# Kernel optimization log

Hardware: AMD Instinct MI355X
Metric: run time of the kernel (lower is better)

The kernel has to match this reference:

```python
import jax, jax.numpy as jnp
import numpy as np

B, N, ATTR = 8, 16384, 14
G, M = 256, 32
ENC = 1024
DIM, DEPTH, HEADS = 384, 12, 6
HID = 4 * DIM
FETCH = (3, 7, 11)


def setup_inputs() -> dict:
    key = jax.random.key(0)
    ks = iter(jax.random.split(key, 40))
    def rn(shape, s=0.02):
        return jax.random.normal(next(ks), shape, dtype=jnp.float32) * s
    inp = {}
    inp["xyz"] = jax.random.normal(next(ks), (B, N, ATTR), dtype=jnp.float32)
    # T-Net: 6 -> 64 -> 512 -> 36 (6x6 transform)
    inp["tn_c1_w"] = rn((64, 6));    inp["tn_c1_b"] = jnp.zeros((64,), jnp.float32)
    inp["tn_bn1_g"] = jnp.ones((64,), jnp.float32);  inp["tn_bn1_b"] = jnp.zeros((64,), jnp.float32)
    inp["tn_c2_w"] = rn((512, 64));  inp["tn_c2_b"] = jnp.zeros((512,), jnp.float32)
    inp["tn_bn2_g"] = jnp.ones((512,), jnp.float32); inp["tn_bn2_b"] = jnp.zeros((512,), jnp.float32)
    inp["tn_fc_w"] = rn((36, 512));  inp["tn_fc_b"] = jnp.zeros((36,), jnp.float32)
    # PointNet encoder: ATTR -> 128 -> 256 -> 512 -> ENC (1x1 convs)
    for i, (o, c) in enumerate([(128, ATTR), (256, 128), (512, 256), (ENC, 512)], 1):
        inp[f"e_c{i}_w"] = rn((o, c)); inp[f"e_c{i}_b"] = jnp.zeros((o,), jnp.float32)
        inp[f"e_bn{i}_g"] = jnp.ones((o,), jnp.float32); inp[f"e_bn{i}_b"] = jnp.zeros((o,), jnp.float32)
    inp["reduce_w"] = rn((DIM, ENC)); inp["reduce_b"] = jnp.zeros((DIM,), jnp.float32)
    inp["pos1_w"] = rn((128, 3));     inp["pos1_b"] = jnp.zeros((128,), jnp.float32)
    inp["pos2_w"] = rn((DIM, 128));   inp["pos2_b"] = jnp.zeros((DIM,), jnp.float32)
    # transformer blocks, stacked over depth
    inp["ln1_g"] = jnp.ones((DEPTH, DIM), jnp.float32); inp["ln1_b"] = jnp.zeros((DEPTH, DIM), jnp.float32)
    inp["qkv_w"] = rn((DEPTH, 3 * DIM, DIM))
    inp["proj_w"] = rn((DEPTH, DIM, DIM)); inp["proj_b"] = jnp.zeros((DEPTH, DIM), jnp.float32)
    inp["ln2_g"] = jnp.ones((DEPTH, DIM), jnp.float32); inp["ln2_b"] = jnp.zeros((DEPTH, DIM), jnp.float32)
    inp["fc1_w"] = rn((DEPTH, HID, DIM)); inp["fc1_b"] = jnp.zeros((DEPTH, HID), jnp.float32)
    inp["fc2_w"] = rn((DEPTH, DIM, HID)); inp["fc2_b"] = jnp.zeros((DEPTH, DIM), jnp.float32)
    return inp


def _bn(x, g, b, eps=1e-5):
    # training-mode BatchNorm1d over [batch, length, channel]
    m = jnp.mean(x, axis=(0, 1))
    v = jnp.var(x, axis=(0, 1))
    return (x - m) * jax.lax.rsqrt(v + eps) * g + b


def _lnorm(x, g, b, eps=1e-5):
    m = jnp.mean(x, axis=-1, keepdims=True)
    v = jnp.var(x, axis=-1, keepdims=True)
    return (x - m) * jax.lax.rsqrt(v + eps) * g + b


def _fps(xyz, npoint):
    # sequential farthest point sampling (deterministic start at index 0)
    b, n, _ = xyz.shape
    coords = xyz[:, :, :3]
    bidx = jnp.arange(b)
    def step(carry, _):
        dist, far = carry
        c = coords[bidx, far]                                   # [B,3]
        d = jnp.sum((coords - c[:, None, :]) ** 2, axis=-1)     # [B,N]
        dist = jnp.minimum(dist, d)
        return (dist, jnp.argmax(dist, axis=-1)), far
    init = (jnp.full((b, n), 1e10, jnp.float32), jnp.zeros((b,), jnp.int32))
    _, idxs = jax.lax.scan(step, init, None, length=npoint)
    return jnp.transpose(idxs)                                   # [B,npoint]


def _forward(xyz, tn_c1_w, tn_c1_b, tn_bn1_g, tn_bn1_b, tn_c2_w, tn_c2_b, tn_bn2_g, tn_bn2_b,
             tn_fc_w, tn_fc_b,
             e_c1_w, e_c1_b, e_bn1_g, e_bn1_b, e_c2_w, e_c2_b, e_bn2_g, e_bn2_b,
             e_c3_w, e_c3_b, e_bn3_g, e_bn3_b, e_c4_w, e_c4_b, e_bn4_g, e_bn4_b,
             reduce_w, reduce_b, pos1_w, pos1_b, pos2_w, pos2_b,
             ln1_g, ln1_b, qkv_w, proj_w, proj_b, ln2_g, ln2_b,
             fc1_w, fc1_b, fc2_w, fc2_b):
    b = xyz.shape[0]
    # ---- grouping: FPS + attribute-space KNN (cdist over all A attrs) ----
    cidx = _fps(xyz, G)                                          # [B,G]
    cattrs = jnp.take_along_axis(xyz, cidx[:, :, None], axis=1)  # [B,G,A]
    center = cattrs[:, :, :3]                                    # [B,G,3]
    d2 = (jnp.sum(cattrs ** 2, -1)[:, :, None] + jnp.sum(xyz ** 2, -1)[:, None, :]
          - 2.0 * jnp.einsum('bga,bna->bgn', cattrs, xyz))       # [B,G,N]
    _, knn = jax.lax.top_k(-d2, M)                               # [B,G,M] smallest dists
    nb = jnp.take_along_axis(xyz, knn.reshape(b, G * M)[:, :, None], axis=1)
    nb = nb.reshape(b, G, M, ATTR)
    nb = jnp.concatenate([nb[..., :3] - center[:, :, None, :], nb[..., 3:]], axis=-1)
    # ---- PointNet encoder with 6x6 T-Net on the first 6 attributes ----
    pg = nb.reshape(b * G, M, ATTR)
    x6 = pg[:, :, :6]
    h = jax.nn.relu(_bn(jnp.einsum('bmc,oc->bmo', x6, tn_c1_w) + tn_c1_b, tn_bn1_g, tn_bn1_b))
    h = jax.nn.relu(_bn(jnp.einsum('bmc,oc->bmo', h, tn_c2_w) + tn_c2_b, tn_bn2_g, tn_bn2_b))
    h = jnp.max(h, axis=1)                                       # [BG,512]
    t = (h @ tn_fc_w.T + tn_fc_b + jnp.eye(6, dtype=jnp.float32).reshape(36)).reshape(-1, 6, 6)
    pg = jnp.concatenate([jnp.einsum('bmc,bck->bmk', x6, t), pg[:, :, 6:]], axis=-1)
    p = jax.nn.relu(_bn(jnp.einsum('bmc,oc->bmo', pg, e_c1_w) + e_c1_b, e_bn1_g, e_bn1_b))
    p = jax.nn.relu(_bn(jnp.einsum('bmc,oc->bmo', p, e_c2_w) + e_c2_b, e_bn2_g, e_bn2_b))
    p = jax.nn.relu(_bn(jnp.einsum('bmc,oc->bmo', p, e_c3_w) + e_c3_b, e_bn3_g, e_bn3_b))
    p = _bn(jnp.einsum('bmc,oc->bmo', p, e_c4_w) + e_c4_b, e_bn4_g, e_bn4_b)
    tokens = jnp.max(p, axis=1).reshape(b, G, ENC)               # [B,G,ENC]
    # ---- transformer over group tokens, pos added each layer ----
    x = tokens @ reduce_w.T + reduce_b                           # [B,G,DIM]
    pos = jax.nn.gelu(center @ pos1_w.T + pos1_b) @ pos2_w.T + pos2_b
    scale = (DIM // HEADS) ** -0.5
    feats = []
    for i in range(DEPTH):
        h_in = x + pos
        y = _lnorm(h_in, ln1_g[i], ln1_b[i])
        qkv = jnp.einsum('bnc,oc->bno', y, qkv_w[i]).reshape(b, G, 3, HEADS, DIM // HEADS)
        q, k, v = jnp.moveaxis(qkv, 2, 0)                        # each [B,G,H,D]
        a = jax.nn.softmax(jnp.einsum('bnhd,bmhd->bhnm', q, k) * scale, axis=-1)
        o = jnp.einsum('bhnm,bmhd->bnhd', a, v).reshape(b, G, DIM)
        x = h_in + (jnp.einsum('bnc,oc->bno', o, proj_w[i]) + proj_b[i])
        y = _lnorm(x, ln2_g[i], ln2_b[i])
        y = jax.nn.gelu(jnp.einsum('bnc,oc->bno', y, fc1_w[i]) + fc1_b[i])
        x = x + (jnp.einsum('bnc,oc->bno', y, fc2_w[i]) + fc2_b[i])
        if i in FETCH:
            feats.append(x)
    return jnp.stack(feats)                                      # [3,B,G,DIM]


def reference(xyz, tn_c1_w, tn_c1_b, tn_bn1_g, tn_bn1_b, tn_c2_w, tn_c2_b, tn_bn2_g, tn_bn2_b,
              tn_fc_w, tn_fc_b,
              e_c1_w, e_c1_b, e_bn1_g, e_bn1_b, e_c2_w, e_c2_b, e_bn2_g, e_bn2_b,
              e_c3_w, e_c3_b, e_bn3_g, e_bn3_b, e_c4_w, e_c4_b, e_bn4_g, e_bn4_b,
              reduce_w, reduce_b, pos1_w, pos1_b, pos2_w, pos2_b,
              ln1_g, ln1_b, qkv_w, proj_w, proj_b, ln2_g, ln2_b,
              fc1_w, fc1_b, fc2_w, fc2_b):
    return _forward(xyz, tn_c1_w, tn_c1_b, tn_bn1_g, tn_bn1_b, tn_c2_w, tn_c2_b, tn_bn2_g, tn_bn2_b,
                    tn_fc_w, tn_fc_b,
                    e_c1_w, e_c1_b, e_bn1_g, e_bn1_b, e_c2_w, e_c2_b, e_bn2_g, e_bn2_b,
                    e_c3_w, e_c3_b, e_bn3_g, e_bn3_b, e_c4_w, e_c4_b, e_bn4_g, e_bn4_b,
                    reduce_w, reduce_b, pos1_w, pos1_b, pos2_w, pos2_b,
                    ln1_g, ln1_b, qkv_w, proj_w, proj_b, ln2_g, ln2_b,
                    fc1_w, fc1_b, fc2_w, fc2_b)
```

## Files before the change

kernel.cpp:

```cpp
#include <hip/hip_runtime.h>
#include <hip/hip_bf16.h>
#include <math.h>

typedef __hip_bfloat16 bf16;
typedef __attribute__((ext_vector_type(8))) short bfrag;
typedef __attribute__((ext_vector_type(4))) float f32x4;

constexpr int B_ = 8, N_ = 16384, ATTR_ = 14, G_ = 256, M_ = 32;
constexpr int BG = B_ * G_;
constexpr int ROWS = BG * M_;
constexpr int DIM_ = 384, HEADS_ = 6;

static inline int cdiv(int a, int b) { return (a + b - 1) / b; }

__device__ __forceinline__ float gelu_f(float x) {
  float x3 = x * x * x;
  float t = tanhf(0.7978845608028654f * (x + 0.044715f * x3));
  return 0.5f * x * (1.0f + t);
}

__global__ __launch_bounds__(1024) void fps_kernel(const float* __restrict__ xyz,
                                                   int* __restrict__ cidx) {
  const int b = blockIdx.x;
  const int tid = threadIdx.x;
  const float* base = xyz + (size_t)b * N_ * ATTR_;
  float px[16], py[16], pz[16], dist[16];
#pragma unroll
  for (int j = 0; j < 16; ++j) {
    int n = tid + j * 1024;
    px[j] = base[(size_t)n * ATTR_ + 0];
    py[j] = base[(size_t)n * ATTR_ + 1];
    pz[j] = base[(size_t)n * ATTR_ + 2];
    dist[j] = 1e10f;
  }
  __shared__ float s_v[16];
  __shared__ int s_i[16];
  __shared__ int s_far;
  int far = 0;
  for (int g = 0; g < G_; ++g) {
    if (tid == 0) cidx[b * G_ + g] = far;
    float cx = base[(size_t)far * ATTR_ + 0];
    float cy = base[(size_t)far * ATTR_ + 1];
    float cz = base[(size_t)far * ATTR_ + 2];
    float best = -1.0f; int bi = 0;
#pragma unroll
    for (int j = 0; j < 16; ++j) {
      float dx = __fsub_rn(px[j], cx);
      float dy = __fsub_rn(py[j], cy);
      float dz = __fsub_rn(pz[j], cz);
      float d = __fadd_rn(__fadd_rn(__fmul_rn(dx, dx), __fmul_rn(dy, dy)), __fmul_rn(dz, dz));
      float nd = fminf(dist[j], d);
      dist[j] = nd;
      int n = tid + j * 1024;
      if (nd > best) { best = nd; bi = n; }
    }
    for (int off = 32; off > 0; off >>= 1) {
      float ov = __shfl_down(best, off);
      int   oi = __shfl_down(bi, off);
      if (ov > best || (ov == best && oi < bi)) { best = ov; bi = oi; }
    }
    if ((tid & 63) == 0) { s_v[tid >> 6] = best; s_i[tid >> 6] = bi; }
    __syncthreads();
    if (tid == 0) {
      float bv = s_v[0]; int bj = s_i[0];
      for (int w = 1; w < 16; ++w)
        if (s_v[w] > bv || (s_v[w] == bv && s_i[w] < bj)) { bv = s_v[w]; bj = s_i[w]; }
      s_far = bj;
    }
    __syncthreads();
    far = s_far;
  }
}

__global__ void pn2_kernel(const float* __restrict__ xyz, float* __restrict__ pn2) {
  int gid = blockIdx.x * blockDim.x + threadIdx.x;
  if (gid >= B_ * N_) return;
  const float* p = xyz + (size_t)gid * ATTR_;
  float s = 0.f;
#pragma unroll
  for (int a = 0; a < ATTR_; ++a) s = __fadd_rn(s, __fmul_rn(p[a], p[a]));
  pn2[gid] = s;
}

__global__ __launch_bounds__(256) void knn_kernel(const float* __restrict__ xyz,
                                                  const float* __restrict__ pn2,
                                                  const int* __restrict__ cidx,
                                                  int* __restrict__ knn) {
  const int bg = blockIdx.x;
  const int b = bg >> 8;
  const int tid = threadIdx.x;
  __shared__ float d2s[N_];
  __shared__ float catt[ATTR_];
  __shared__ float lv[256]; __shared__ int li[256];
  __shared__ float rv[256]; __shared__ int ri[256];
  const float* xb = xyz + (size_t)b * N_ * ATTR_;
  if (tid == 0) {
    int ci = cidx[bg];
    for (int a = 0; a < ATTR_; ++a) catt[a] = xb[(size_t)ci * ATTR_ + a];
  }
  __syncthreads();
  float cn2 = 0.f;
#pragma unroll
  for (int a = 0; a < ATTR_; ++a) cn2 = __fadd_rn(cn2, __fmul_rn(catt[a], catt[a]));
  const float* pnb = pn2 + (size_t)b * N_;
  const int base = tid * 64;
  float bv = 3.0e38f; int bi = 0;
  for (int j = 0; j < 64; ++j) {
    int n = base + j;
    const float* p = xb + (size_t)n * ATTR_;
    float dot = 0.f;
#pragma unroll
    for (int a = 0; a < ATTR_; ++a) dot = __fadd_rn(dot, __fmul_rn(catt[a], p[a]));
    float v = __fsub_rn(__fadd_rn(cn2, pnb[n]), __fmul_rn(2.0f, dot));
    d2s[n] = v;
    if (v < bv) { bv = v; bi = n; }
  }
  lv[tid] = bv; li[tid] = bi;
  __syncthreads();
  for (int m = 0; m < M_; ++m) {
    rv[tid] = lv[tid]; ri[tid] = li[tid];
    __syncthreads();
    for (int s = 128; s > 0; s >>= 1) {
      if (tid < s) {
        float ov = rv[tid + s]; int oi = ri[tid + s];
        if (ov < rv[tid] || (ov == rv[tid] && oi < ri[tid])) { rv[tid] = ov; ri[tid] = oi; }
      }
      __syncthreads();
    }
    int win = ri[0];
    if (tid == 0) knn[(size_t)bg * M_ + m] = win;
    if (tid == (win >> 6)) {
      d2s[win] = 3.0e38f;
      float nbv = 3.0e38f; int nbi = 0;
      for (int j = 0; j < 64; ++j) {
        int n = base + j;
        float v = d2s[n];
        if (v < nbv) { nbv = v; nbi = n; }
      }
      lv[tid] = nbv; li[tid] = nbi;
    }
    __syncthreads();
  }
}

__global__ void pg_build_kernel(const float* __restrict__ xyz, const int* __restrict__ cidx,
                                const int* __restrict__ knn, float* __restrict__ pg,
                                float* __restrict__ center) {
  int gid = blockIdx.x * blockDim.x + threadIdx.x;
  if (gid >= ROWS) return;
  int bg = gid >> 5, mm = gid & 31;
  int b = bg >> 8;
  int ci = cidx[bg];
  int ni = knn[(size_t)bg * M_ + mm];
  const float* c = xyz + ((size_t)b * N_ + ci) * ATTR_;
  const float* p = xyz + ((size_t)b * N_ + ni) * ATTR_;
  float* o = pg + (size_t)gid * ATTR_;
#pragma unroll
  for (int a = 0; a < 3; ++a) o[a] = __fsub_rn(p[a], c[a]);
#pragma unroll
  for (int a = 3; a < ATTR_; ++a) o[a] = p[a];
  if (mm == 0) {
    center[bg * 3 + 0] = c[0]; center[bg * 3 + 1] = c[1]; center[bg * 3 + 2] = c[2];
  }
}

template<bool ABF, bool BIAS, bool GELUE, bool EYE, bool OBF>
__global__ __launch_bounds__(256) void gemm_kernel(
    const void* __restrict__ Ap, const float* __restrict__ W,
    const float* __restrict__ bias, void* __restrict__ Cp,
    int Mrows, int K, int OC, int lda) {
  __shared__ float As[16][68];
  __shared__ float Ws[16][68];
  const int tid = threadIdx.x;
  const int tx = tid & 15, ty = tid >> 4;
  const int row0 = blockIdx.y * 64, col0 = blockIdx.x * 64;
  float acc[4][4] = {{0.f}};
  const float* Af = (const float*)Ap;
  const bf16* Ab = (const bf16*)Ap;
  const int r = tid >> 2;
  const int kb = (tid & 3) * 4;
  for (int k0 = 0; k0 < K; k0 += 16) {
#pragma unroll
    for (int i = 0; i < 4; ++i) {
      int kk = kb + i, kg = k0 + kk;
      float a = 0.f, w = 0.f;
      if (kg < K) {
        size_t ai = (size_t)(row0 + r) * lda + kg;
        a = ABF ? __bfloat162float(Ab[ai]) : Af[ai];
        int oc = col0 + r;
        if (oc < OC) w = W[(size_t)oc * K + kg];
      }
      As[kk][r] = a;
      Ws[kk][r] = w;
    }
    __syncthreads();
#pragma unroll
    for (int kk = 0; kk < 16; ++kk) {
      float av[4], bv[4];
#pragma unroll
      for (int i = 0; i < 4; ++i) av[i] = As[kk][ty * 4 + i];
#pragma unroll
      for (int j = 0; j < 4; ++j) bv[j] = Ws[kk][tx * 4 + j];
#pragma unroll
      for (int i = 0; i < 4; ++i)
#pragma unroll
        for (int j = 0; j < 4; ++j) acc[i][j] = fmaf(av[i], bv[j], acc[i][j]);
    }
    __syncthreads();
  }
#pragma unroll
  for (int i = 0; i < 4; ++i) {
    int row = row0 + ty * 4 + i;
#pragma unroll
    for (int j = 0; j < 4; ++j) {
      int c = col0 + tx * 4 + j;
      if (c >= OC) continue;
      float v = acc[i][j];
      if (BIAS) v += bias[c];
      if (EYE) { if ((c / 6) == (c % 6)) v += 1.0f; }
      if (GELUE) v = gelu_f(v);
      size_t oi = (size_t)row * OC + c;
      if (OBF) ((bf16*)Cp)[oi] = __float2bfloat16(v);
      else ((float*)Cp)[oi] = v;
    }
  }
}

template<int BM, int BN, bool WF32, bool BIAS, bool GELUE, bool RES, bool OBF>
__global__ __launch_bounds__(256) void mfma_gemm(
    const bf16* __restrict__ A, const void* __restrict__ Wp,
    const float* __restrict__ bias, const float* __restrict__ res,
    void* __restrict__ Cp, int K, int OC) {
  constexpr int MR = BM / 32;
  constexpr int NR = BN / 32;
  __shared__ __align__(16) bf16 As[BM * 64];
  __shared__ __align__(16) bf16 Ws[BN * 64];
  const int tid = threadIdx.x;
  const int wid = tid >> 6, lane = tid & 63;
  const int wm = wid >> 1, wn = wid & 1;
  const int l15 = lane & 15, l4 = lane >> 4;
  const int row0 = blockIdx.y * BM, col0 = blockIdx.x * BN;
  const float* Wf = (const float*)Wp;
  const bf16* Wb = (const bf16*)Wp;
  f32x4 acc[MR][NR];
#pragma unroll
  for (int m = 0; m < MR; ++m)
#pragma unroll
    for (int n = 0; n < NR; ++n) acc[m][n] = (f32x4){0.f, 0.f, 0.f, 0.f};

  for (int k0 = 0; k0 < K; k0 += 64) {
#pragma unroll
    for (int t = tid; t < BM * 8; t += 256) {
      int r = t >> 3, c = t & 7;
      uint4 v = *(const uint4*)(A + (size_t)(row0 + r) * K + k0 + c * 8);
      *(uint4*)(As + r * 64 + ((c ^ (r & 7)) * 8)) = v;
    }
#pragma unroll
    for (int t = tid; t < BN * 8; t += 256) {
      int r = t >> 3, c = t & 7;
      uint4 v;
      if (WF32) {
        const float* src = Wf + (size_t)(col0 + r) * K + k0 + c * 8;
        float4 f0 = *(const float4*)src;
        float4 f1 = *(const float4*)(src + 4);
        bf16 tmp[8];
        tmp[0] = __float2bfloat16(f0.x); tmp[1] = __float2bfloat16(f0.y);
        tmp[2] = __float2bfloat16(f0.z); tmp[3] = __float2bfloat16(f0.w);
        tmp[4] = __float2bfloat16(f1.x); tmp[5] = __float2bfloat16(f1.y);
        tmp[6] = __float2bfloat16(f1.z); tmp[7] = __float2bfloat16(f1.w);
        v = *(uint4*)tmp;
      } else {
        v = *(const uint4*)(Wb + (size_t)(col0 + r) * K + k0 + c * 8);
      }
      *(uint4*)(Ws + r * 64 + ((c ^ (r & 7)) * 8)) = v;
    }
    __syncthreads();
#pragma unroll
    for (int kk = 0; kk < 2; ++kk) {
      const int chunk = kk * 4 + l4;
      bfrag a[MR], b[NR];
#pragma unroll
      for (int m = 0; m < MR; ++m) {
        int R = wm * (BM / 2) + m * 16 + l15;
        a[m] = *(const bfrag*)(As + R * 64 + ((chunk ^ (R & 7)) * 8));
      }
#pragma unroll
      for (int n = 0; n < NR; ++n) {
        int R = wn * (BN / 2) + n * 16 + l15;
        b[n] = *(const bfrag*)(Ws + R * 64 + ((chunk ^ (R & 7)) * 8));
      }
#pragma unroll
      for (int m = 0; m < MR; ++m)
#pragma unroll
        for (int n = 0; n < NR; ++n)
          acc[m][n] = __builtin_amdgcn_mfma_f32_16x16x32_bf16(a[m], b[n], acc[m][n], 0, 0, 0);
    }
    __syncthreads();
  }
#pragma unroll
  for (int m = 0; m < MR; ++m) {
    int rbase = row0 + wm * (BM / 2) + m * 16 + l4 * 4;
#pragma unroll
    for (int n = 0; n < NR; ++n) {
      int c = col0 + wn * (BN / 2) + n * 16 + l15;
      float bs = BIAS ? bias[c] : 0.f;
#pragma unroll
      for (int j = 0; j < 4; ++j) {
        int row = rbase + j;
        float v = acc[m][n][j] + bs;
        if (GELUE) v = gelu_f(v);
        if (RES) v += res[(size_t)row * OC + c];
        size_t oi = (size_t)row * OC + c;
        if (OBF) ((bf16*)Cp)[oi] = __float2bfloat16(v);
        else ((float*)Cp)[oi] = v;
      }
    }
  }
}

__global__ __launch_bounds__(256) void bn_stats_kernel(const bf16* __restrict__ Y,
                                                       float* __restrict__ stats, int C) {
  const int r0 = blockIdx.x * 256;
  const int tid = threadIdx.x;
  for (int c = tid; c < C; c += 256) {
    float s = 0.f, q = 0.f;
    for (int r = 0; r < 256; ++r) {
      float y = __bfloat162float(Y[(size_t)(r0 + r) * C + c]);
      s += y; q += y * y;
    }
    atomicAdd(&stats[c], s);
    atomicAdd(&stats[C + c], q);
  }
}

__global__ void bn_fin_kernel(const float* __restrict__ stats, const float* __restrict__ g,
                              const float* __restrict__ b, float* __restrict__ ss, int C) {
  int c = blockIdx.x * blockDim.x + threadIdx.x;
  if (c >= C) return;
  const float inv_n = 1.0f / (float)ROWS;
  float m = stats[c] * inv_n;
  float v = stats[C + c] * inv_n - m * m;
  float sc = g[c] * (1.0f / sqrtf(v + 1e-5f));
  ss[c] = sc;
  ss[C + c] = b[c] - m * sc;
}

__global__ __launch_bounds__(256) void bnrelu_kernel(bf16* __restrict__ Y,
                                                     const float* __restrict__ ss,
                                                     int C, int total8) {
  for (int i = blockIdx.x * blockDim.x + threadIdx.x; i < total8; i += gridDim.x * blockDim.x) {
    size_t base = (size_t)i * 8;
    int c0 = (int)(base % (size_t)C);
    uint4 v = *(uint4*)(Y + base);
    bf16* e = (bf16*)&v;
#pragma unroll
    for (int j = 0; j < 8; ++j) {
      float f = fmaf(__bfloat162float(e[j]), ss[c0 + j], ss[C + c0 + j]);
      e[j] = __float2bfloat16(fmaxf(f, 0.f));
    }
    *(uint4*)(Y + base) = v;
  }
}

template<bool RELU, bool OBF>
__global__ void maxpool_kernel(const bf16* __restrict__ Y, const float* __restrict__ ss,
                               void* __restrict__ out, int C) {
  int gid = blockIdx.x * blockDim.x + threadIdx.x;
  if (gid >= BG * C) return;
  int bg = gid / C, c = gid - bg * C;
  float sc = ss[c], sh = ss[C + c];
  float m = -3.0e38f;
  for (int j = 0; j < M_; ++j) {
    float y = __bfloat162float(Y[((size_t)bg * M_ + j) * C + c]);
    float v = fmaf(y, sc, sh);
    if (RELU) v = fmaxf(v, 0.f);
    m = fmaxf(m, v);
  }
  if (OBF) ((bf16*)out)[gid] = __float2bfloat16(m);
  else ((float*)out)[gid] = m;
}

__global__ void tnet_apply_kernel(const float* __restrict__ pg, const float* __restrict__ tmat,
                                  float* __restrict__ pg2) {
  int row = blockIdx.x * blockDim.x + threadIdx.x;
  if (row >= ROWS) return;
  int bg = row >> 5;
  const float* t = tmat + (size_t)bg * 36;
  const float* in = pg + (size_t)row * ATTR_;
  float* o = pg2 + (size_t)row * ATTR_;
  float x[6];
#pragma unroll
  for (int c = 0; c < 6; ++c) x[c] = in[c];
#pragma unroll
  for (int k = 0; k < 6; ++k) {
    float s = 0.f;
#pragma unroll
    for (int c = 0; c < 6; ++c) s = fmaf(x[c], t[c * 6 + k], s);
    o[k] = s;
  }
#pragma unroll
  for (int a = 6; a < ATTR_; ++a) o[a] = in[a];
}

template<bool ADDPOS>
__global__ __launch_bounds__(128) void ln_kernel(const float* __restrict__ x,
                                                 const float* __restrict__ pos,
                                                 const float* __restrict__ g,
                                                 const float* __restrict__ b,
                                                 float* __restrict__ hin,
                                                 bf16* __restrict__ y) {
  const int row = blockIdx.x;
  const int tid = threadIdx.x;
  float v[3];
  float s = 0.f;
#pragma unroll
  for (int i = 0; i < 3; ++i) {
    int c = tid + i * 128;
    float t = x[(size_t)row * DIM_ + c];
    if (ADDPOS) t += pos[(size_t)row * DIM_ + c];
    v[i] = t; s += t;
  }
  for (int off = 32; off > 0; off >>= 1) s += __shfl_down(s, off);
  __shared__ float sa[2], sb[2];
  if ((tid & 63) == 0) sa[tid >> 6] = s;
  __syncthreads();
  float mean = (sa[0] + sa[1]) * (1.0f / DIM_);
  float q = 0.f;
#pragma unroll
  for (int i = 0; i < 3; ++i) { float d = v[i] - mean; q += d * d; }
  for (int off = 32; off > 0; off >>= 1) q += __shfl_down(q, off);
  if ((tid & 63) == 0) sb[tid >> 6] = q;
  __syncthreads();
  float var = (sb[0] + sb[1]) * (1.0f / DIM_);
  float rs = 1.0f / sqrtf(var + 1e-5f);
#pragma unroll
  for (int i = 0; i < 3; ++i) {
    int c = tid + i * 128;
    if (ADDPOS) hin[(size_t)row * DIM_ + c] = v[i];
    y[(size_t)row * DIM_ + c] = __float2bfloat16(fmaf((v[i] - mean) * rs, g[c], b[c]));
  }
}

__global__ __launch_bounds__(256) void attn_kernel(const float* __restrict__ qkv,
                                                   bf16* __restrict__ obuf) {
  const int blk = blockIdx.x;
  const int qt = blk & 3;
  const int bh = blk >> 2;
  const int b = bh / HEADS_, h = bh % HEADS_;
  const int tid = threadIdx.x;
  __shared__ float Qs[64][65];
  __shared__ float KVs[256][65];
  __shared__ float Ss[64][257];
  const int n0 = qt * 64;
  const size_t qbase = (size_t)b * G_ * (3 * DIM_);
#pragma unroll 4
  for (int i = 0; i < 16; ++i) {
    int idx = i * 256 + tid;
    int qr = idx >> 6, d = idx & 63;
    Qs[qr][d] = qkv[qbase + (size_t)(n0 + qr) * (3 * DIM_) + h * 64 + d];
  }
#pragma unroll 4
  for (int i = 0; i < 64; ++i) {
    int idx = i * 256 + tid;
    int kr = idx >> 6, d = idx & 63;
    KVs[kr][d] = qkv[qbase + (size_t)kr * (3 * DIM_) + DIM_ + h * 64 + d];
  }
  __syncthreads();
  const int q = tid >> 2, kl = tid & 3;
  float lmax = -3.0e38f;
#pragma unroll 4
  for (int kk = 0; kk < 64; ++kk) {
    int k = kl + kk * 4;
    float s = 0.f;
#pragma unroll
    for (int d = 0; d < 64; ++d) s = fmaf(Qs[q][d], KVs[k][d], s);
    s *= 0.125f;
    Ss[q][k] = s;
    lmax = fmaxf(lmax, s);
  }
  lmax = fmaxf(lmax, __shfl_xor(lmax, 1));
  lmax = fmaxf(lmax, __shfl_xor(lmax, 2));
  float lsum = 0.f;
#pragma unroll 4
  for (int kk = 0; kk < 64; ++kk) {
    int k = kl + kk * 4;
    float e = expf(Ss[q][k] - lmax);
    Ss[q][k] = e;
    lsum += e;
  }
  lsum += __shfl_xor(lsum, 1);
  lsum += __shfl_xor(lsum, 2);
#pragma unroll 4
  for (int kk = 0; kk < 64; ++kk) {
    int k = kl + kk * 4;
    Ss[q][k] = Ss[q][k] / lsum;
  }
  __syncthreads();
#pragma unroll 4
  for (int i = 0; i < 64; ++i) {
    int idx = i * 256 + tid;
    int kr = idx >> 6, d = idx & 63;
    KVs[kr][d] = qkv[qbase + (size_t)kr * (3 * DIM_) + 2 * DIM_ + h * 64 + d];
  }
  __syncthreads();
  float oacc[16];
#pragma unroll
  for (int i = 0; i < 16; ++i) oacc[i] = 0.f;
  for (int k = 0; k < 256; ++k) {
    float s = Ss[q][k];
#pragma unroll
    for (int dd = 0; dd < 16; ++dd) oacc[dd] = fmaf(s, KVs[k][kl + dd * 4], oacc[dd]);
  }
  bf16* ob = obuf + (size_t)(b * G_ + n0 + q) * DIM_ + h * 64;
#pragma unroll
  for (int dd = 0; dd < 16; ++dd) ob[kl + dd * 4] = __float2bfloat16(oacc[dd]);
}

extern "C" void kernel_launch(void* const* d_in, const int* in_sizes, int n_in,
                              void* d_out, int out_size, void* d_ws, size_t ws_size,
                              hipStream_t stream) {
  const float* xyz      = (const float*)d_in[0];
  const float* tn_c1_w  = (const float*)d_in[1];
  const float* tn_c1_b  = (const float*)d_in[2];
  const float* tn_bn1_g = (const float*)d_in[3];
  const float* tn_bn1_b = (const float*)d_in[4];
  const float* tn_c2_w  = (const float*)d_in[5];
  const float* tn_c2_b  = (const float*)d_in[6];
  const float* tn_bn2_g = (const float*)d_in[7];
  const float* tn_bn2_b = (const float*)d_in[8];
  const float* tn_fc_w  = (const float*)d_in[9];
  const float* tn_fc_b  = (const float*)d_in[10];
  const float* e_c1_w = (const float*)d_in[11];
  const float* e_c1_b = (const float*)d_in[12];
  const float* e_bn1_g = (const float*)d_in[13];
  const float* e_bn1_b = (const float*)d_in[14];
  const float* e_c2_w = (const float*)d_in[15];
  const float* e_c2_b = (const float*)d_in[16];
  const float* e_bn2_g = (const float*)d_in[17];
  const float* e_bn2_b = (const float*)d_in[18];
  const float* e_c3_w = (const float*)d_in[19];
  const float* e_c3_b = (const float*)d_in[20];
  const float* e_bn3_g = (const float*)d_in[21];
  const float* e_bn3_b = (const float*)d_in[22];
  const float* e_c4_w = (const float*)d_in[23];
  const float* e_c4_b = (const float*)d_in[24];
  const float* e_bn4_g = (const float*)d_in[25];
  const float* e_bn4_b = (const float*)d_in[26];
  const float* reduce_w = (const float*)d_in[27];
  const float* reduce_b = (const float*)d_in[28];
  const float* pos1_w = (const float*)d_in[29];
  const float* pos1_b = (const float*)d_in[30];
  const float* pos2_w = (const float*)d_in[31];
  const float* pos2_b = (const float*)d_in[32];
  const float* ln1_g = (const float*)d_in[33];
  const float* ln1_b = (const float*)d_in[34];
  const float* qkv_w = (const float*)d_in[35];
  const float* proj_w = (const float*)d_in[36];
  const float* proj_b = (const float*)d_in[37];
  const float* ln2_g = (const float*)d_in[38];
  const float* ln2_b = (const float*)d_in[39];
  const float* fc1_w = (const float*)d_in[40];
  const float* fc1_b = (const float*)d_in[41];
  const float* fc2_w = (const float*)d_in[42];
  const float* fc2_b = (const float*)d_in[43];
  (void)in_sizes; (void)n_in; (void)out_size; (void)ws_size;

  char* ws = (char*)d_ws;
  size_t off = 0;
  auto alloc = [&](size_t bytes) -> void* {
    void* p = ws + off;
    off = (off + bytes + 255) & ~(size_t)255;
    return p;
  };

  char* stats_begin = ws + off;
  float* stats_tn1 = (float*)alloc(2 * 64 * 4);
  float* stats_tn2 = (float*)alloc(2 * 512 * 4);
  float* stats_e1 = (float*)alloc(2 * 128 * 4);
  float* stats_e2 = (float*)alloc(2 * 256 * 4);
  float* stats_e3 = (float*)alloc(2 * 512 * 4);
  float* stats_e4 = (float*)alloc(2 * 1024 * 4);
  size_t stats_len = (size_t)((ws + off) - stats_begin);
  float* ss_tn1 = (float*)alloc(2 * 64 * 4);
  float* ss_tn2 = (float*)alloc(2 * 512 * 4);
  float* ss_e1 = (float*)alloc(2 * 128 * 4);
  float* ss_e2 = (float*)alloc(2 * 256 * 4);
  float* ss_e3 = (float*)alloc(2 * 512 * 4);
  float* ss_e4 = (float*)alloc(2 * 1024 * 4);
  int* cidx = (int*)alloc((size_t)BG * 4);
  int* knn = (int*)alloc((size_t)ROWS * 4);
  float* pn2 = (float*)alloc((size_t)B_ * N_ * 4);
  float* center = (float*)alloc((size_t)BG * 3 * 4);
  float* pg = (float*)alloc((size_t)ROWS * ATTR_ * 4);
  float* pg2 = (float*)alloc((size_t)ROWS * ATTR_ * 4);
  float* hmax = (float*)alloc((size_t)BG * 512 * 4);
  float* tmat = (float*)alloc((size_t)BG * 36 * 4);
  bf16* tokens = (bf16*)alloc((size_t)BG * 1024 * 2);
  float* xb = (float*)alloc((size_t)BG * DIM_ * 4);
  float* posb = (float*)alloc((size_t)BG * DIM_ * 4);
  float* hinb = (float*)alloc((size_t)BG * DIM_ * 4);
  bf16* yb = (bf16*)alloc((size_t)BG * DIM_ * 2);
  float* qkvb = (float*)alloc((size_t)BG * 3 * DIM_ * 4);
  bf16* obf = (bf16*)alloc((size_t)BG * DIM_ * 2);
  bf16* hmlp = (bf16*)alloc((size_t)BG * 1536 * 2);
  float* p1 = (float*)alloc((size_t)BG * 128 * 4);
  bf16* Bbuf0 = (bf16*)alloc((size_t)ROWS * 512 * 2);
  bf16* Bbuf1 = (bf16*)alloc((size_t)ROWS * 1024 * 2);

  hipMemsetAsync(stats_begin, 0, stats_len, stream);

  fps_kernel<<<B_, 1024, 0, stream>>>(xyz, cidx);
  pn2_kernel<<<cdiv(B_ * N_, 256), 256, 0, stream>>>(xyz, pn2);
  knn_kernel<<<BG, 256, 0, stream>>>(xyz, pn2, cidx, knn);
  pg_build_kernel<<<cdiv(ROWS, 256), 256, 0, stream>>>(xyz, cidx, knn, pg, center);

  gemm_kernel<false, true, false, false, true>
      <<<dim3(1, ROWS / 64), 256, 0, stream>>>(pg, tn_c1_w, tn_c1_b, Bbuf0, ROWS, 6, 64, ATTR_);
  bn_stats_kernel<<<ROWS / 256, 256, 0, stream>>>(Bbuf0, stats_tn1, 64);
  bn_fin_kernel<<<1, 64, 0, stream>>>(stats_tn1, tn_bn1_g, tn_bn1_b, ss_tn1, 64);
  bnrelu_kernel<<<2048, 256, 0, stream>>>(Bbuf0, ss_tn1, 64, ROWS * 64 / 8);
  mfma_gemm<128, 128, true, true, false, false, true>
      <<<dim3(4, ROWS / 128), 256, 0, stream>>>(Bbuf0, tn_c2_w, tn_c2_b, nullptr, Bbuf1, 64, 512);
  bn_stats_kernel<<<ROWS / 256, 256, 0, stream>>>(Bbuf1, stats_tn2, 512);
  bn_fin_kernel<<<2, 256, 0, stream>>>(stats_tn2, tn_bn2_g, tn_bn2_b, ss_tn2, 512);
  maxpool_kernel<true, false><<<cdiv(BG * 512, 256), 256, 0, stream>>>(Bbuf1, ss_tn2, hmax, 512);
  gemm_kernel<false, true, false, true, false>
      <<<dim3(1, BG / 64), 256, 0, stream>>>(hmax, tn_fc_w, tn_fc_b, tmat, BG, 512, 36, 512);
  tnet_apply_kernel<<<cdiv(ROWS, 256), 256, 0, stream>>>(pg, tmat, pg2);

  gemm_kernel<false, true, false, false, true>
      <<<dim3(2, ROWS / 64), 256, 0, stream>>>(pg2, e_c1_w, e_c1_b, Bbuf0, ROWS, ATTR_, 128, ATTR_);
  bn_stats_kernel<<<ROWS / 256, 256, 0, stream>>>(Bbuf0, stats_e1, 128);
  bn_fin_kernel<<<1, 128, 0, stream>>>(stats_e1, e_bn1_g, e_bn1_b, ss_e1, 128);
  bnrelu_kernel<<<2048, 256, 0, stream>>>(Bbuf0, ss_e1, 128, ROWS * 128 / 8);
  mfma_gemm<128, 128, true, true, false, false, true>
      <<<dim3(2, ROWS / 128), 256, 0, stream>>>(Bbuf0, e_c2_w, e_c2_b, nullptr, Bbuf1, 128, 256);
  bn_stats_kernel<<<ROWS / 256, 256, 0, stream>>>(Bbuf1, stats_e2, 256);
  bn_fin_kernel<<<1, 256, 0, stream>>>(stats_e2, e_bn2_g, e_bn2_b, ss_e2, 256);
  bnrelu_kernel<<<2048, 256, 0, stream>>>(Bbuf1, ss_e2, 256, ROWS * 256 / 8);
  mfma_gemm<128, 128, true, true, false, false, true>
      <<<dim3(4, ROWS / 128), 256, 0, stream>>>(Bbuf1, e_c3_w, e_c3_b, nullptr, Bbuf0, 256, 512);
  bn_stats_kernel<<<ROWS / 256, 256, 0, stream>>>(Bbuf0, stats_e3, 512);
  bn_fin_kernel<<<2, 256, 0, stream>>>(stats_e3, e_bn3_g, e_bn3_b, ss_e3, 512);
  bnrelu_kernel<<<2048, 256, 0, stream>>>(Bbuf0, ss_e3, 512, ROWS * 512 / 8);
  mfma_gemm<128, 128, true, true, false, false, true>
      <<<dim3(8, ROWS / 128), 256, 0, stream>>>(Bbuf0, e_c4_w, e_c4_b, nullptr, Bbuf1, 512, 1024);
  bn_stats_kernel<<<ROWS / 256, 256, 0, stream>>>(Bbuf1, stats_e4, 1024);
  bn_fin_kernel<<<4, 256, 0, stream>>>(stats_e4, e_bn4_g, e_bn4_b, ss_e4, 1024);
  maxpool_kernel<false, true><<<cdiv(BG * 1024, 256), 256, 0, stream>>>(Bbuf1, ss_e4, tokens, 1024);

  mfma_gemm<64, 64, true, true, false, false, false>
      <<<dim3(6, BG / 64), 256, 0, stream>>>(tokens, reduce_w, reduce_b, nullptr, xb, 1024, DIM_);
  gemm_kernel<false, true, true, false, false>
      <<<dim3(2, BG / 64), 256, 0, stream>>>(center, pos1_w, pos1_b, p1, BG, 3, 128, 3);
  gemm_kernel<false, true, false, false, false>
      <<<dim3(6, BG / 64), 256, 0, stream>>>(p1, pos2_w, pos2_b, posb, BG, 128, DIM_, 128);

  int slot = 0;
  for (int i = 0; i < 12; ++i) {
    ln_kernel<true><<<BG, 128, 0, stream>>>(xb, posb, ln1_g + (size_t)i * DIM_,
                                            ln1_b + (size_t)i * DIM_, hinb, yb);
    mfma_gemm<64, 128, true, false, false, false, false>
        <<<dim3(9, BG / 64), 256, 0, stream>>>(yb, qkv_w + (size_t)i * 3 * DIM_ * DIM_,
                                               nullptr, nullptr, qkvb, DIM_, 3 * DIM_);
    attn_kernel<<<B_ * HEADS_ * 4, 256, 0, stream>>>(qkvb, obf);
    mfma_gemm<64, 64, true, true, false, true, false>
        <<<dim3(6, BG / 64), 256, 0, stream>>>(obf, proj_w + (size_t)i * DIM_ * DIM_,
                                               proj_b + (size_t)i * DIM_, hinb, xb, DIM_, DIM_);
    ln_kernel<false><<<BG, 128, 0, stream>>>(xb, nullptr, ln2_g + (size_t)i * DIM_,
                                             ln2_b + (size_t)i * DIM_, nullptr, yb);
    mfma_gemm<64, 128, true, true, true, false, true>
        <<<dim3(12, BG / 64), 256, 0, stream>>>(yb, fc1_w + (size_t)i * 1536 * DIM_,
                                                fc1_b + (size_t)i * 1536, nullptr, hmlp,
                                                DIM_, 1536);
    mfma_gemm<64, 64, true, true, false, true, false>
        <<<dim3(6, BG / 64), 256, 0, stream>>>(hmlp, fc2_w + (size_t)i * DIM_ * 1536,
                                               fc2_b + (size_t)i * DIM_, xb, xb, 1536, DIM_);
    if (i == 3 || i == 7 || i == 11) {
      hipMemcpyAsync((float*)d_out + (size_t)slot * BG * DIM_, xb,
                     (size_t)BG * DIM_ * 4, hipMemcpyDeviceToDevice, stream);
      ++slot;
    }
  }
}
```

Baseline: 4.766 ms.

## Use wave-local top-k selection in KNN and broadcast FPS centroid coordinates

In the KNN kernel, the 32-step block-wide shared-memory reduction with many __syncthreads is replaced. Each wave now independently finds its own 32 smallest distances using xor-shuffles, and one thread merges the four sorted per-wave lists. In FPS, every thread reduces the 16 per-wave candidates redundantly, and the thread that owns the winning point writes its coordinates to shared memory. This removes the serial tid-0 step and the dependent global reload of the centroid. The cost is redundant per-wave work and a serial 4-way merge by a single thread.

```diff
diff --git a/kernel.cpp b/kernel.cpp
--- a/kernel.cpp
+++ b/kernel.cpp
@@ -35,13 +35,11 @@
   }
   __shared__ float s_v[16];
   __shared__ int s_i[16];
-  __shared__ int s_far;
+  __shared__ float s_cx, s_cy, s_cz;
   int far = 0;
+  float cx = base[0], cy = base[1], cz = base[2];
   for (int g = 0; g < G_; ++g) {
     if (tid == 0) cidx[b * G_ + g] = far;
-    float cx = base[(size_t)far * ATTR_ + 0];
-    float cy = base[(size_t)far * ATTR_ + 1];
-    float cz = base[(size_t)far * ATTR_ + 2];
     float best = -1.0f; int bi = 0;
 #pragma unroll
     for (int j = 0; j < 16; ++j) {
@@ -54,6 +52,7 @@
       int n = tid + j * 1024;
       if (nd > best) { best = nd; bi = n; }
     }
+#pragma unroll
     for (int off = 32; off > 0; off >>= 1) {
       float ov = __shfl_down(best, off);
       int   oi = __shfl_down(bi, off);
@@ -61,14 +60,22 @@
     }
     if ((tid & 63) == 0) { s_v[tid >> 6] = best; s_i[tid >> 6] = bi; }
     __syncthreads();
-    if (tid == 0) {
-      float bv = s_v[0]; int bj = s_i[0];
-      for (int w = 1; w < 16; ++w)
-        if (s_v[w] > bv || (s_v[w] == bv && s_i[w] < bj)) { bv = s_v[w]; bj = s_i[w]; }
-      s_far = bj;
+    float bv = s_v[0]; int win = s_i[0];
+#pragma unroll
+    for (int w = 1; w < 16; ++w) {
+      float v = s_v[w]; int iw = s_i[w];
+      if (v > bv || (v == bv && iw < win)) { bv = v; win = iw; }
+    }
+    if (tid == (win & 1023)) {
+      int jw = win >> 10;
+      float wx = px[0], wy = py[0], wz = pz[0];
+#pragma unroll
+      for (int j = 1; j < 16; ++j)
+        if (j == jw) { wx = px[j]; wy = py[j]; wz = pz[j]; }
+      s_cx = wx; s_cy = wy; s_cz = wz;
     }
     __syncthreads();
-    far = s_far;
+    far = win; cx = s_cx; cy = s_cy; cz = s_cz;
   }
 }
 
@@ -89,10 +96,11 @@
   const int bg = blockIdx.x;
   const int b = bg >> 8;
   const int tid = threadIdx.x;
+  const int wave = tid >> 6, lane = tid & 63;
   __shared__ float d2s[N_];
   __shared__ float catt[ATTR_];
-  __shared__ float lv[256]; __shared__ int li[256];
-  __shared__ float rv[256]; __shared__ int ri[256];
+  __shared__ float wv[4][32];
+  __shared__ int wi[4][32];
   const float* xb = xyz + (size_t)b * N_ * ATTR_;
   if (tid == 0) {
     int ci = cidx[bg];
@@ -115,31 +123,41 @@
     d2s[n] = v;
     if (v < bv) { bv = v; bi = n; }
   }
-  lv[tid] = bv; li[tid] = bi;
+  for (int m = 0; m < M_; ++m) {
+    float v = bv; int i = bi;
+#pragma unroll
+    for (int off = 1; off < 64; off <<= 1) {
+      float ov = __shfl_xor(v, off);
+      int   oi = __shfl_xor(i, off);
+      if (ov < v || (ov == v && oi < i)) { v = ov; i = oi; }
+    }
+    if (lane == 0) { wv[wave][m] = v; wi[wave][m] = i; }
+    if (i >= base && i < base + 64) {
+      d2s[i] = 3.0e38f;
+      bv = 3.0e38f; bi = base;
+#pragma unroll 4
+      for (int jj = 0; jj < 16; ++jj) {
+        float4 q4 = *(const float4*)(d2s + base + jj * 4);
+        int n0 = base + jj * 4;
+        if (q4.x < bv) { bv = q4.x; bi = n0; }
+        if (q4.y < bv) { bv = q4.y; bi = n0 + 1; }
+        if (q4.z < bv) { bv = q4.z; bi = n0 + 2; }
+        if (q4.w < bv) { bv = q4.w; bi = n0 + 3; }
+      }
+    }
+  }
   __syncthreads();
-  for (int m = 0; m < M_; ++m) {
-    rv[tid] = lv[tid]; ri[tid] = li[tid];
-    __syncthreads();
-    for (int s = 128; s > 0; s >>= 1) {
-      if (tid < s) {
-        float ov = rv[tid + s]; int oi = ri[tid + s];
-        if (ov < rv[tid] || (ov == rv[tid] && oi < ri[tid])) { rv[tid] = ov; ri[tid] = oi; }
-      }
-      __syncthreads();
-    }
-    int win = ri[0];
-    if (tid == 0) knn[(size_t)bg * M_ + m] = win;
-    if (tid == (win >> 6)) {
-      d2s[win] = 3.0e38f;
-      float nbv = 3.0e38f; int nbi = 0;
-      for (int j = 0; j < 64; ++j) {
-        int n = base + j;
-        float v = d2s[n];
-        if (v < nbv) { nbv = v; nbi = n; }
-      }
-      lv[tid] = nbv; li[tid] = nbi;
-    }
-    __syncthreads();
+  if (tid == 0) {
+    int h0 = 0, h1 = 0, h2 = 0, h3 = 0;
+    for (int m = 0; m < M_; ++m) {
+      float mv = 3.0e38f; int midx = 0x7fffffff; int mw = 0;
+      if (h0 < 32) { float v = wv[0][h0]; int ix = wi[0][h0]; if (v < mv || (v == mv && ix < midx)) { mv = v; midx = ix; mw = 0; } }
+      if (h1 < 32) { float v = wv[1][h1]; int ix = wi[1][h1]; if (v < mv || (v == mv && ix < midx)) { mv = v; midx = ix; mw = 1; } }
+      if (h2 < 32) { float v = wv[2][h2]; int ix = wi[2][h2]; if (v < mv || (v == mv && ix < midx)) { mv = v; midx = ix; mw = 2; } }
+      if (h3 < 32) { float v = wv[3][h3]; int ix = wi[3][h3]; if (v < mv || (v == mv && ix < midx)) { mv = v; midx = ix; mw = 3; } }
+      knn[(size_t)bg * M_ + m] = midx;
+      if (mw == 0) ++h0; else if (mw == 1) ++h1; else if (mw == 2) ++h2; else ++h3;
+    }
   }
 }
 
```

Measured after the change: 4.791 ms. About the same (+0.5%).
